# Optimization experiments

Measured on AMD Instinct MI355X. Metric: run time of the kernel, lower is better.

## Reference

```python
import jax, jax.numpy as jnp
import numpy as np

N, E, F, C = 100000, 1600000, 64, 256


def setup_inputs() -> dict:
    key = jax.random.key(0)
    ks = jax.random.split(key, 9)

    def lin(k, fi, fo):
        kw, kb = jax.random.split(k)
        w = jax.random.normal(kw, (fi, fo), jnp.float32) * np.float32(1.0 / np.sqrt(fi))
        b = jax.random.normal(kb, (fo,), jnp.float32) * 0.001
        return w, b

    content = jax.random.normal(ks[0], (N, C), jnp.float32)
    node_emb = jax.random.normal(ks[1], (N + 1, F), jnp.float32) * np.float32(1.0 / (100 * F))
    proj_w, proj_b = lin(ks[2], C, F)
    c0w1, c0b1 = lin(ks[3], 2 * F, 4 * F)   # first layer: inp=2F -> 4F
    c0w2, c0b2 = lin(ks[4], 4 * F, F)
    c1w1, c1b1 = lin(ks[5], 3 * F, 6 * F)   # prediction layer: inp=3F -> 6F
    c1w2, c1b2 = lin(ks[6], 6 * F, F)
    nid = jnp.arange(N, dtype=jnp.int32)
    src = jax.random.randint(ks[7], (E,), 0, N, dtype=jnp.int32)
    dst = jax.random.randint(ks[8], (E,), 0, N, dtype=jnp.int32)
    return dict(content=content, node_emb=node_emb, proj_w=proj_w, proj_b=proj_b,
                c0w1=c0w1, c0b1=c0b1, c0w2=c0w2, c0b2=c0b2,
                c1w1=c1w1, c1b1=c1b1, c1w2=c1w2, c1b2=c1b2,
                nid=nid, src=src, dst=dst)


def _l2norm(x):
    # per-node L2 renorm with clamp(min=1e-6) like torch .norm().clamp
    n = jnp.linalg.norm(x, axis=1, keepdims=True)
    return x / jnp.maximum(n, 1e-6)


def _forward(content, node_emb, proj_w, proj_b,
             c0w1, c0b1, c0w2, c0b2, c1w1, c1b1, c1w2, c1b2,
             nid, src, dst):
    n = content.shape[0]
    lrelu = lambda x: jax.nn.leaky_relu(x, 0.1)
    # node init: embedding + projected content (GaussianNoise is identity in eval)
    h = node_emb[nid + 1] + lrelu(content @ proj_w + proj_b)
    # w = sum of 'one' over in-neighbors = in-degree
    deg = jax.ops.segment_sum(jnp.ones(src.shape[0], h.dtype), dst, num_segments=n)
    wden = jnp.maximum(deg - 1.0, 1.0)[:, None]  # (w - 1).clamp(min=1)

    # ---- layer 0 (first_layer) ----
    h_agg = jax.ops.segment_sum(h[src], dst, num_segments=n)  # copy_src('h') + sum
    h_agg = (h_agg - h) / wden
    z = lrelu(jnp.concatenate([h, h_agg], axis=1) @ c0w1 + c0b1)
    h_new = _l2norm(lrelu(z @ c0w2 + c0b2))
    h_res = _l2norm(h_agg)  # skip is None since in_dims == out_dims
    h = h_new

    # ---- layer 1 (prediction_layer) ----
    h_agg = jax.ops.segment_sum(h[src], dst, num_segments=n)
    h_res_sum = jax.ops.segment_sum(h_res[src], dst, num_segments=n)
    h_agg = (h_agg - h) / wden
    z = lrelu(jnp.concatenate([h, h_agg, h_res_sum], axis=1) @ c1w1 + c1b1)
    h_new = z @ c1w2 + c1b2  # prediction layer: no trailing LeakyReLU
    return _l2norm(h_new)


def reference(content, node_emb, proj_w, proj_b, c0w1, c0b1, c0w2, c0b2,
              c1w1, c1b1, c1w2, c1b2, nid, src, dst):
    return _forward(content, node_emb, proj_w, proj_b,
                    c0w1, c0b1, c0w2, c0b2, c1w1, c1b1, c1w2, c1b2,
                    nid, src, dst)
```

## Files before the change

kernel.cpp:

```cpp
#include <hip/hip_runtime.h>

typedef _Float16 half_t;
typedef half_t h8 __attribute__((ext_vector_type(8)));
typedef float f32x4 __attribute__((ext_vector_type(4)));
typedef unsigned int uint;
typedef unsigned long long ull;
typedef unsigned short ushort;

__device__ __forceinline__ float lrelu_f(float x){ return x >= 0.f ? x : 0.1f*x; }

__device__ __forceinline__ float2 unpack_h2(uint v){
  half_t lo = __builtin_bit_cast(half_t, (unsigned short)(v & 0xffffu));
  half_t hi = __builtin_bit_cast(half_t, (unsigned short)(v >> 16));
  return make_float2((float)lo, (float)hi);
}
__device__ __forceinline__ uint pack_h2(float a, float b){
  unsigned short lo = __builtin_bit_cast(unsigned short, (half_t)a);
  unsigned short hi = __builtin_bit_cast(unsigned short, (half_t)b);
  return (uint)lo | ((uint)hi << 16);
}
__device__ __forceinline__ h8 as_h8(uint4 v){ return __builtin_bit_cast(h8, v); }

enum { EPI_INIT=0, EPI_LRELU=1, EPI_LRELU_L2=2, EPI_L2=3 };
constexpr int CAP = 64;
constexpr int CHUNK = 4096;
constexpr int OSTR = 1056;

__global__ void pack_all_kernel(const float* __restrict__ s0, half_t* __restrict__ d0,
                                const float* __restrict__ s1, half_t* __restrict__ d1,
                                const float* __restrict__ s2, half_t* __restrict__ d2,
                                const float* __restrict__ s3, half_t* __restrict__ d3,
                                const float* __restrict__ s4, half_t* __restrict__ d4){
  int b = blockIdx.x;
  const float* w; half_t* o; int K, M;
  if      (b < 8)  { w=s0; o=d0; K=256; M=64;  }
  else if (b < 24) { w=s1; o=d1; K=128; M=256; b-=8; }
  else if (b < 32) { w=s2; o=d2; K=256; M=64;  b-=24; }
  else if (b < 68) { w=s3; o=d3; K=192; M=384; b-=32; }
  else             { w=s4; o=d4; K=384; M=64;  b-=68; }
  int idx = b*256 + threadIdx.x;
  int total = (K/32)*(M/16)*64;
  if (idx >= total) return;
  int lane = idx & 63;
  int t = idx >> 6;
  int CBn = M/16;
  int cb = t % CBn;
  int s  = t / CBn;
  int k0 = s*32 + (lane>>4)*8;
  int c  = cb*16 + (lane&15);
  #pragma unroll
  for (int j=0;j<8;++j) o[(size_t)idx*8 + j] = (half_t)w[(size_t)(k0+j)*M + c];
}

__global__ __launch_bounds__(256) void binA_kernel(const int* __restrict__ src, const int* __restrict__ dst,
    ull* __restrict__ staging, ushort* __restrict__ offs, int E, int nb){
  __shared__ int hist[1024];
  __shared__ int cursor[1024];
  int c = blockIdx.x;
  int base = c * CHUNK;
  for (int j = threadIdx.x; j < 1024; j += 256) hist[j] = 0;
  __syncthreads();
  #pragma unroll
  for (int it=0; it<CHUNK/256; ++it){
    int i = base + it*256 + threadIdx.x;
    if (i < E) atomicAdd(&hist[dst[i] >> 7], 1);
  }
  __syncthreads();
  for (int off=1; off<1024; off<<=1){
    int v[4];
    #pragma unroll
    for (int k=0;k<4;++k){
      int j = threadIdx.x + k*256;
      v[k] = (j>=off)? hist[j-off] : 0;
    }
    __syncthreads();
    #pragma unroll
    for (int k=0;k<4;++k) hist[threadIdx.x + k*256] += v[k];
    __syncthreads();
  }
  for (int j = threadIdx.x; j < 1024; j += 256){
    int ex = j ? hist[j-1] : 0;
    cursor[j] = ex;
    if (j <= nb) offs[(size_t)c*OSTR + j] = (ushort)ex;
  }
  __syncthreads();
  #pragma unroll
  for (int it=0; it<CHUNK/256; ++it){
    int i = base + it*256 + threadIdx.x;
    if (i < E){
      int d = dst[i];
      int s = src[i];
      int pos = atomicAdd(&cursor[d >> 7], 1);
      staging[(size_t)c*CHUNK + pos] = ((ull)(uint)d << 32) | (uint)s;
    }
  }
}

__global__ __launch_bounds__(256) void scatB_kernel(const ull* __restrict__ staging,
    const ushort* __restrict__ offs, int* __restrict__ cnt, int* __restrict__ col,
    int nChunks, int n){
  __shared__ int lcnt[128];
  int b = blockIdx.x;
  int node0 = b << 7;
  if (threadIdx.x < 128) lcnt[threadIdx.x] = 0;
  __syncthreads();
  for (int c = threadIdx.x; c < nChunks; c += 256){
    const ushort* op = offs + (size_t)c*OSTR;
    int o0 = op[b], o1 = op[b+1];
    const ull* sp = staging + (size_t)c*CHUNK;
    for (int j = o0; j < o1; ++j){
      ull v = sp[j];
      int d = (int)(v >> 32);
      int s = (int)(uint)v;
      int r = atomicAdd(&lcnt[d & 127], 1);
      if (r < CAP) col[(size_t)d*CAP + r] = s;
    }
  }
  __syncthreads();
  if (threadIdx.x < 128){
    int node = node0 + threadIdx.x;
    if (node < n) cnt[node] = lcnt[threadIdx.x];
  }
}

template<int K, int MOUT, int EPI>
__global__ __launch_bounds__(256) void gemm_kernel(
  const float* __restrict__ x0, int st0,
  const half_t* __restrict__ wp, const float* __restrict__ bias,
  half_t* __restrict__ outv, int ost,
  const float* __restrict__ emb, const int* __restrict__ nid, int n)
{
  constexpr int KS = K/32;
  constexpr int CB = MOUT/16;
  const int lane = threadIdx.x & 63;
  const int wid  = threadIdx.x >> 6;
  const int row0 = blockIdx.x*64 + wid*16;
  const int arow = row0 + (lane & 15);
  const int arowc = arow < n ? arow : n-1;
  const int khi = (lane>>4)*8;

  f32x4 areg[2*KS];
  #pragma unroll
  for (int s=0;s<KS;++s){
    int k0 = s*32 + khi;
    areg[2*s]   = *(const f32x4*)(x0 + (size_t)arowc*st0 + k0);
    areg[2*s+1] = *(const f32x4*)(x0 + (size_t)arowc*st0 + k0 + 4);
  }

  f32x4 acc[CB];
  #pragma unroll
  for (int cb=0;cb<CB;++cb) acc[cb] = (f32x4){0.f,0.f,0.f,0.f};

  #pragma unroll
  for (int s=0;s<KS;++s){
    h8 af;
    #pragma unroll
    for (int j=0;j<4;++j){ af[j]=(half_t)areg[2*s][j]; af[j+4]=(half_t)areg[2*s+1][j]; }
    const h8* wrow = (const h8*)wp + (size_t)(s*CB)*64 + lane;
    #pragma unroll
    for (int cb=0;cb<CB;++cb){
      h8 bf = wrow[cb*64];
      acc[cb] = __builtin_amdgcn_mfma_f32_16x16x32_f16(af, bf, acc[cb], 0,0,0);
    }
  }

  const int cgrp = lane >> 4;
  const int ccol = lane & 15;
  #pragma unroll
  for (int r=0;r<4;++r){
    int R = row0 + cgrp*4 + r;
    if (R < n){
      #pragma unroll
      for (int cb=0;cb<CB;++cb){
        float t = lrelu_f(acc[cb][r] + bias[cb*16+ccol]);
        if constexpr (EPI==EPI_INIT) t += emb[(size_t)(nid[R]+1)*64 + cb*16 + ccol];
        outv[(size_t)R*ost + cb*16 + ccol] = (half_t)t;
      }
    }
  }
}

template<int K1, int M1, int M2, int NSRC, int EPI2, bool OUTF16>
__global__ __launch_bounds__(256,4) void mlp_kernel(
  const half_t* __restrict__ x0, const half_t* __restrict__ x1, const half_t* __restrict__ x2,
  int st0, int st1, int st2,
  const half_t* __restrict__ wp1, const float* __restrict__ b1,
  const half_t* __restrict__ wp2, const float* __restrict__ b2,
  void* __restrict__ outv, int ost, int n)
{
  constexpr int RS  = 17;
  constexpr int KS1 = K1/32, CBT = M1/16, CBW = CBT/4;
  constexpr int KS2 = M1/32, CB2 = M2/16;
  constexpr int RED = 65;
  __shared__ uint  zc[M1*RS];
  __shared__ float red[2*16*RED];

  const int lane = threadIdx.x & 63;
  const int wid  = threadIdx.x >> 6;
  const int row0 = blockIdx.x*32;
  const int khi  = (lane>>4)*8;
  const int ccol = lane & 15;
  const int cgrp = lane >> 4;

  f32x4 acc[2][CBW];
  #pragma unroll
  for (int t=0;t<2;++t)
    #pragma unroll
    for (int cb=0;cb<CBW;++cb) acc[t][cb] = (f32x4){0.f,0.f,0.f,0.f};

  #pragma unroll
  for (int s=0;s<KS1;++s){
    int k0 = s*32 + khi;
    const half_t* p = x0; int st = st0; int koff = k0;
    if constexpr (NSRC>1){
      int isrc = k0 >> 6;
      if constexpr (NSRC>=2){ if (isrc==1){ p=x1; st=st1; } }
      if constexpr (NSRC>=3){ if (isrc==2){ p=x2; st=st2; } }
      koff = k0 & 63;
    }
    h8 af[2];
    #pragma unroll
    for (int t=0;t<2;++t){
      int ar = row0 + t*16 + ccol; if (ar >= n) ar = n-1;
      af[t] = *(const h8*)(p + (size_t)ar*st + koff);
    }
    #pragma unroll
    for (int cb=0;cb<CBW;++cb){
      h8 bf = ((const h8*)wp1)[(size_t)(s*CBT + wid*CBW + cb)*64 + lane];
      #pragma unroll
      for (int t=0;t<2;++t)
        acc[t][cb] = __builtin_amdgcn_mfma_f32_16x16x32_f16(af[t], bf, acc[t][cb], 0,0,0);
    }
  }
  #pragma unroll
  for (int t=0;t<2;++t){
    #pragma unroll
    for (int cb=0;cb<CBW;++cb){
      int col = wid*(CBW*16) + cb*16 + ccol;
      float bb = b1[col];
      float v0 = lrelu_f(acc[t][cb][0]+bb);
      float v1 = lrelu_f(acc[t][cb][1]+bb);
      float v2 = lrelu_f(acc[t][cb][2]+bb);
      float v3 = lrelu_f(acc[t][cb][3]+bb);
      int idx = col*RS + t*8 + cgrp*2;
      zc[idx]   = pack_h2(v0,v1);
      zc[idx+1] = pack_h2(v2,v3);
    }
  }
  __syncthreads();

  const int rt = wid & 1, kh = wid >> 1;
  f32x4 acc2[CB2];
  #pragma unroll
  for (int cb=0;cb<CB2;++cb) acc2[cb] = (f32x4){0.f,0.f,0.f,0.f};
  const uint sel = (lane&1) ? 0x07060302u : 0x05040100u;
  const int rp0 = rt*8 + (ccol>>1);

  #pragma unroll
  for (int si=0;si<KS2/2;++si){
    int s = kh*(KS2/2) + si;
    uint v[8];
    #pragma unroll
    for (int j=0;j<8;++j) v[j] = zc[(s*32 + khi + j)*RS + rp0];
    uint4 u;
    u.x = __builtin_amdgcn_perm(v[1], v[0], sel);
    u.y = __builtin_amdgcn_perm(v[3], v[2], sel);
    u.z = __builtin_amdgcn_perm(v[5], v[4], sel);
    u.w = __builtin_amdgcn_perm(v[7], v[6], sel);
    h8 af2 = __builtin_bit_cast(h8, u);
    #pragma unroll
    for (int cb=0;cb<CB2;++cb){
      h8 bf = ((const h8*)wp2)[(size_t)(s*CB2+cb)*64 + lane];
      acc2[cb] = __builtin_amdgcn_mfma_f32_16x16x32_f16(af2, bf, acc2[cb], 0,0,0);
    }
  }
  if (kh == 1){
    #pragma unroll
    for (int cb=0;cb<CB2;++cb)
      #pragma unroll
      for (int r=0;r<4;++r)
        red[(rt*16 + cgrp*4 + r)*RED + cb*16 + ccol] = acc2[cb][r];
  }
  __syncthreads();
  if (kh == 0){
    #pragma unroll
    for (int r=0;r<4;++r){
      int Rr = row0 + rt*16 + cgrp*4 + r;
      float vv[CB2];
      #pragma unroll
      for (int cb=0;cb<CB2;++cb){
        float t = acc2[cb][r] + red[(rt*16 + cgrp*4 + r)*RED + cb*16 + ccol] + b2[cb*16+ccol];
        if constexpr (EPI2==EPI_LRELU_L2) t = lrelu_f(t);
        vv[cb] = t;
      }
      float sq = 0.f;
      #pragma unroll
      for (int cb=0;cb<CB2;++cb) sq += vv[cb]*vv[cb];
      sq += __shfl_xor(sq,1); sq += __shfl_xor(sq,2);
      sq += __shfl_xor(sq,4); sq += __shfl_xor(sq,8);
      float inv = 1.f / fmaxf(sqrtf(sq), 1e-6f);
      if (Rr < n){
        #pragma unroll
        for (int cb=0;cb<CB2;++cb){
          float t = vv[cb]*inv;
          if constexpr (OUTF16)
            ((half_t*)outv)[(size_t)Rr*ost + cb*16 + ccol] = (half_t)t;
          else
            ((float*)outv)[(size_t)Rr*ost + cb*16 + ccol] = t;
        }
      }
    }
  }
}

__global__ __launch_bounds__(256) void segsum0_kernel(const uint* __restrict__ hu, const int* __restrict__ cnt,
                               const int* __restrict__ col,
                               uint* __restrict__ hagg, uint* __restrict__ hc, int n){
  int node = blockIdx.x*4 + (threadIdx.x>>6);
  if (node >= n) return;
  int lane = threadIdx.x & 63;
  int g = lane >> 3, l = lane & 7;
  int deg = cnt[node];
  int degc = deg < CAP ? deg : CAP;
  const int* cv = col + (size_t)node*CAP;
  float a[8] = {0,0,0,0,0,0,0,0};
  int j = g;
  for (; j + 8 < degc; j += 16){
    int c0 = cv[j], c1 = cv[j+8];
    uint4 v0 = *(const uint4*)(hu + (size_t)c0*32 + l*4);
    uint4 v1 = *(const uint4*)(hu + (size_t)c1*32 + l*4);
    h8 s = as_h8(v0) + as_h8(v1);
    #pragma unroll
    for (int q=0;q<8;++q) a[q] += (float)s[q];
  }
  if (j < degc){
    int c = cv[j];
    uint4 v = *(const uint4*)(hu + (size_t)c*32 + l*4);
    h8 s = as_h8(v);
    #pragma unroll
    for (int q=0;q<8;++q) a[q] += (float)s[q];
  }
  #pragma unroll
  for (int q=0;q<8;++q){
    a[q] += __shfl_xor(a[q], 8);
    a[q] += __shfl_xor(a[q], 16);
    a[q] += __shfl_xor(a[q], 32);
  }
  uint4 hv4 = *(const uint4*)(hu + (size_t)node*32 + l*4);
  h8 hvh = as_h8(hv4);
  float iwd = 1.f / fmaxf((float)deg - 1.f, 1.f);
  float sq = 0.f;
  #pragma unroll
  for (int q=0;q<8;++q){ a[q] = (a[q]-(float)hvh[q])*iwd; sq += a[q]*a[q]; }
  sq += __shfl_xor(sq,1); sq += __shfl_xor(sq,2); sq += __shfl_xor(sq,4);
  float inv = 1.f / fmaxf(sqrtf(sq), 1e-6f);
  if (g == 0){
    uint4 oa, oh;
    oa.x = pack_h2(a[0],a[1]); oa.y = pack_h2(a[2],a[3]);
    oa.z = pack_h2(a[4],a[5]); oa.w = pack_h2(a[6],a[7]);
    oh.x = pack_h2(a[0]*inv,a[1]*inv); oh.y = pack_h2(a[2]*inv,a[3]*inv);
    oh.z = pack_h2(a[4]*inv,a[5]*inv); oh.w = pack_h2(a[6]*inv,a[7]*inv);
    *(uint4*)(hagg + (size_t)node*32 + l*4) = oa;
    *(uint4*)(hc + (size_t)node*64 + 32 + l*4) = oh;
  }
}

__global__ __launch_bounds__(256) void segsum1_kernel(const uint* __restrict__ hcu, const int* __restrict__ cnt,
                               const int* __restrict__ col,
                               uint* __restrict__ hagg, uint* __restrict__ hsum, int n){
  int node = blockIdx.x*4 + (threadIdx.x>>6);
  if (node >= n) return;
  int lane = threadIdx.x & 63;
  int g = lane >> 4, l = lane & 15;
  int deg = cnt[node];
  int degc = deg < CAP ? deg : CAP;
  const int* cv = col + (size_t)node*CAP;
  float a[8] = {0,0,0,0,0,0,0,0};
  int j = g;
  for (; j + 12 < degc; j += 16){
    int c0 = cv[j], c1 = cv[j+4], c2 = cv[j+8], c3 = cv[j+12];
    uint4 v0 = *(const uint4*)(hcu + (size_t)c0*64 + l*4);
    uint4 v1 = *(const uint4*)(hcu + (size_t)c1*64 + l*4);
    uint4 v2 = *(const uint4*)(hcu + (size_t)c2*64 + l*4);
    uint4 v3 = *(const uint4*)(hcu + (size_t)c3*64 + l*4);
    h8 s = (as_h8(v0) + as_h8(v1)) + (as_h8(v2) + as_h8(v3));
    #pragma unroll
    for (int q=0;q<8;++q) a[q] += (float)s[q];
  }
  for (; j < degc; j += 4){
    int c = cv[j];
    uint4 v = *(const uint4*)(hcu + (size_t)c*64 + l*4);
    h8 s = as_h8(v);
    #pragma unroll
    for (int q=0;q<8;++q) a[q] += (float)s[q];
  }
  #pragma unroll
  for (int q=0;q<8;++q){
    a[q] += __shfl_xor(a[q], 16);
    a[q] += __shfl_xor(a[q], 32);
  }
  if (g == 0){
    if (l < 8){
      uint4 hv4 = *(const uint4*)(hcu + (size_t)node*64 + l*4);
      h8 hvh = as_h8(hv4);
      float iwd = 1.f / fmaxf((float)deg - 1.f, 1.f);
      uint4 o;
      o.x = pack_h2((a[0]-(float)hvh[0])*iwd,(a[1]-(float)hvh[1])*iwd);
      o.y = pack_h2((a[2]-(float)hvh[2])*iwd,(a[3]-(float)hvh[3])*iwd);
      o.z = pack_h2((a[4]-(float)hvh[4])*iwd,(a[5]-(float)hvh[5])*iwd);
      o.w = pack_h2((a[6]-(float)hvh[6])*iwd,(a[7]-(float)hvh[7])*iwd);
      *(uint4*)(hagg + (size_t)node*32 + l*4) = o;
    } else {
      uint4 o;
      o.x = pack_h2(a[0],a[1]); o.y = pack_h2(a[2],a[3]);
      o.z = pack_h2(a[4],a[5]); o.w = pack_h2(a[6],a[7]);
      *(uint4*)(hsum + (size_t)node*32 + (l-8)*4) = o;
    }
  }
}

extern "C" void kernel_launch(void* const* d_in, const int* in_sizes, int n_in,
                              void* d_out, int out_size, void* d_ws, size_t ws_size,
                              hipStream_t stream){
  const float* content = (const float*)d_in[0];
  const float* node_emb= (const float*)d_in[1];
  const float* proj_w  = (const float*)d_in[2];
  const float* proj_b  = (const float*)d_in[3];
  const float* c0w1 = (const float*)d_in[4];
  const float* c0b1 = (const float*)d_in[5];
  const float* c0w2 = (const float*)d_in[6];
  const float* c0b2 = (const float*)d_in[7];
  const float* c1w1 = (const float*)d_in[8];
  const float* c1b1 = (const float*)d_in[9];
  const float* c1w2 = (const float*)d_in[10];
  const float* c1b2 = (const float*)d_in[11];
  const int* nid = (const int*)d_in[12];
  const int* src = (const int*)d_in[13];
  const int* dst = (const int*)d_in[14];
  float* out = (float*)d_out;
  const int n = in_sizes[12];
  const int E = in_sizes[13];

  char* ws = (char*)d_ws;
  size_t off = 0;
  auto alloc = [&](size_t bytes)->char*{
    char* p = ws + off;
    off = (off + bytes + 255) & ~(size_t)255;
    return p;
  };
  const int nChunks = (E + CHUNK - 1)/CHUNK;
  const int nb = (n + 127) >> 7;
  half_t* h0   = (half_t*)alloc((size_t)n*64*2);
  half_t* hc   = (half_t*)alloc((size_t)n*128*2);
  half_t* hagg0= (half_t*)alloc((size_t)n*64*2);
  half_t* hagg1= (half_t*)alloc((size_t)n*64*2);
  half_t* hsum1= (half_t*)alloc((size_t)n*64*2);
  int* cnt    = (int*)alloc((size_t)n*4);
  int* col    = (int*)alloc((size_t)n*CAP*4);
  ull* staging= (ull*)alloc((size_t)nChunks*CHUNK*8);
  ushort* offs= (ushort*)alloc((size_t)nChunks*OSTR*2);
  half_t* wp0 = (half_t*)alloc((size_t)256*64*2);
  half_t* wp1 = (half_t*)alloc((size_t)128*256*2);
  half_t* wp2 = (half_t*)alloc((size_t)256*64*2);
  half_t* wp3 = (half_t*)alloc((size_t)192*384*2);
  half_t* wp4 = (half_t*)alloc((size_t)384*64*2);

  pack_all_kernel<<<80,256,0,stream>>>(proj_w, wp0, c0w1, wp1, c0w2, wp2, c1w1, wp3, c1w2, wp4);

  binA_kernel<<<nChunks,256,0,stream>>>(src, dst, staging, offs, E, nb);
  scatB_kernel<<<nb,256,0,stream>>>(staging, offs, cnt, col, nChunks, n);

  const int rgrid = (n + 63)/64;
  const int mgrid = (n + 31)/32;

  gemm_kernel<256,64,EPI_INIT><<<rgrid,256,0,stream>>>(
      content, 256, wp0, proj_b, h0, 64, node_emb, nid, n);

  segsum0_kernel<<<(n+3)/4,256,0,stream>>>((const uint*)h0, cnt, col,
                                           (uint*)hagg0, (uint*)hc, n);
  mlp_kernel<128,256,64,2,EPI_LRELU_L2,true><<<mgrid,256,0,stream>>>(
      h0, hagg0, nullptr, 64,64,0, wp1, c0b1, wp2, c0b2, hc, 128, n);

  segsum1_kernel<<<(n+3)/4,256,0,stream>>>((const uint*)hc, cnt, col,
                                           (uint*)hagg1, (uint*)hsum1, n);
  mlp_kernel<192,384,64,3,EPI_L2,false><<<mgrid,256,0,stream>>>(
      hc, hagg1, hsum1, 128,64,64, wp3, c1b1, wp4, c1b2, out, 64, n);
}
```

Measured before the change: 278.1 us.

## Fuse neighbor aggregation into MLP kernels via shared-memory tiles

Removes the two separate segment-sum kernels and performs the neighbor gather and reduction inside each MLP kernel for its 32-row tile. The aggregated rows (and the residual sum in layer 1) go to an LDS tile that overlays the existing reduction buffer, and the first GEMM reads them from there. This drops the global writes and re-reads of hagg0, hagg1 and hsum1, and saves two kernel launches. In exchange, each wave now walks 8 nodes one after another before its MFMA work, which may reduce the parallelism available for the gather.

```diff
diff --git a/kernel.cpp b/kernel.cpp
--- a/kernel.cpp
+++ b/kernel.cpp
@@ -9,11 +9,6 @@
 
 __device__ __forceinline__ float lrelu_f(float x){ return x >= 0.f ? x : 0.1f*x; }
 
-__device__ __forceinline__ float2 unpack_h2(uint v){
-  half_t lo = __builtin_bit_cast(half_t, (unsigned short)(v & 0xffffu));
-  half_t hi = __builtin_bit_cast(half_t, (unsigned short)(v >> 16));
-  return make_float2((float)lo, (float)hi);
-}
 __device__ __forceinline__ uint pack_h2(float a, float b){
   unsigned short lo = __builtin_bit_cast(unsigned short, (half_t)a);
   unsigned short hi = __builtin_bit_cast(unsigned short, (half_t)b);
@@ -180,20 +175,29 @@
   }
 }
 
-template<int K1, int M1, int M2, int NSRC, int EPI2, bool OUTF16>
-__global__ __launch_bounds__(256,4) void mlp_kernel(
-  const half_t* __restrict__ x0, const half_t* __restrict__ x1, const half_t* __restrict__ x2,
-  int st0, int st1, int st2,
+template<int GL, int K1, int M1, int M2, int EPI2, bool OUTF16>
+__global__ __launch_bounds__(256,4) void mlpf_kernel(
+  const half_t* __restrict__ x0, int st0,
+  const uint* __restrict__ gsrc,
+  const int* __restrict__ cnt, const int* __restrict__ col,
   const half_t* __restrict__ wp1, const float* __restrict__ b1,
   const half_t* __restrict__ wp2, const float* __restrict__ b2,
-  void* __restrict__ outv, int ost, int n)
+  void* __restrict__ outv, int ost,
+  uint* __restrict__ hresOut, int n)
 {
   constexpr int RS  = 17;
+  constexpr int RSA = 72;
   constexpr int KS1 = K1/32, CBT = M1/16, CBW = CBT/4;
   constexpr int KS2 = M1/32, CB2 = M2/16;
   constexpr int RED = 65;
+  constexpr int TILEB = (GL==0 ? 1 : 2)*32*RSA*2;
+  constexpr int REDB  = 2*16*RED*4;
+  constexpr int OVLB  = TILEB > REDB ? TILEB : REDB;
   __shared__ uint  zc[M1*RS];
-  __shared__ float red[2*16*RED];
+  __shared__ uint4 ovl[(OVLB+15)/16];
+  half_t* haggT = (half_t*)ovl;
+  half_t* hsumT = (half_t*)ovl + 32*RSA;
+  float*  red   = (float*)ovl;
 
   const int lane = threadIdx.x & 63;
   const int wid  = threadIdx.x >> 6;
@@ -202,6 +206,111 @@
   const int ccol = lane & 15;
   const int cgrp = lane >> 4;
 
+  if constexpr (GL==0){
+    const int g8 = lane >> 3, l8 = lane & 7;
+    for (int pass=0; pass<8; ++pass){
+      int node = row0 + pass*4 + wid;
+      if (node < n){
+        int deg = cnt[node];
+        int degc = deg < CAP ? deg : CAP;
+        const int* cv = col + (size_t)node*CAP;
+        float a[8] = {0,0,0,0,0,0,0,0};
+        int j = g8;
+        for (; j + 8 < degc; j += 16){
+          int c0 = cv[j], c1 = cv[j+8];
+          uint4 v0 = *(const uint4*)(gsrc + (size_t)c0*32 + l8*4);
+          uint4 v1 = *(const uint4*)(gsrc + (size_t)c1*32 + l8*4);
+          h8 s = as_h8(v0) + as_h8(v1);
+          #pragma unroll
+          for (int q=0;q<8;++q) a[q] += (float)s[q];
+        }
+        if (j < degc){
+          uint4 v = *(const uint4*)(gsrc + (size_t)cv[j]*32 + l8*4);
+          h8 s = as_h8(v);
+          #pragma unroll
+          for (int q=0;q<8;++q) a[q] += (float)s[q];
+        }
+        #pragma unroll
+        for (int q=0;q<8;++q){
+          a[q] += __shfl_xor(a[q], 8);
+          a[q] += __shfl_xor(a[q], 16);
+          a[q] += __shfl_xor(a[q], 32);
+        }
+        uint4 hv4 = *(const uint4*)(gsrc + (size_t)node*32 + l8*4);
+        h8 hvh = as_h8(hv4);
+        float iwd = 1.f / fmaxf((float)deg - 1.f, 1.f);
+        float sq = 0.f;
+        #pragma unroll
+        for (int q=0;q<8;++q){ a[q] = (a[q]-(float)hvh[q])*iwd; sq += a[q]*a[q]; }
+        sq += __shfl_xor(sq,1); sq += __shfl_xor(sq,2); sq += __shfl_xor(sq,4);
+        float inv = 1.f / fmaxf(sqrtf(sq), 1e-6f);
+        if (g8 == 0){
+          int lrow = pass*4 + wid;
+          uint4 oa, oh;
+          oa.x = pack_h2(a[0],a[1]); oa.y = pack_h2(a[2],a[3]);
+          oa.z = pack_h2(a[4],a[5]); oa.w = pack_h2(a[6],a[7]);
+          oh.x = pack_h2(a[0]*inv,a[1]*inv); oh.y = pack_h2(a[2]*inv,a[3]*inv);
+          oh.z = pack_h2(a[4]*inv,a[5]*inv); oh.w = pack_h2(a[6]*inv,a[7]*inv);
+          *(uint4*)(haggT + (size_t)lrow*RSA + l8*8) = oa;
+          *(uint4*)(hresOut + (size_t)node*64 + 32 + l8*4) = oh;
+        }
+      }
+    }
+  } else {
+    const int g16 = lane >> 4, l16 = lane & 15;
+    for (int pass=0; pass<8; ++pass){
+      int node = row0 + pass*4 + wid;
+      if (node < n){
+        int deg = cnt[node];
+        int degc = deg < CAP ? deg : CAP;
+        const int* cv = col + (size_t)node*CAP;
+        float a[8] = {0,0,0,0,0,0,0,0};
+        int j = g16;
+        for (; j + 12 < degc; j += 16){
+          int c0 = cv[j], c1 = cv[j+4], c2 = cv[j+8], c3 = cv[j+12];
+          uint4 v0 = *(const uint4*)(gsrc + (size_t)c0*64 + l16*4);
+          uint4 v1 = *(const uint4*)(gsrc + (size_t)c1*64 + l16*4);
+          uint4 v2 = *(const uint4*)(gsrc + (size_t)c2*64 + l16*4);
+          uint4 v3 = *(const uint4*)(gsrc + (size_t)c3*64 + l16*4);
+          h8 s = (as_h8(v0) + as_h8(v1)) + (as_h8(v2) + as_h8(v3));
+          #pragma unroll
+          for (int q=0;q<8;++q) a[q] += (float)s[q];
+        }
+        for (; j < degc; j += 4){
+          uint4 v = *(const uint4*)(gsrc + (size_t)cv[j]*64 + l16*4);
+          h8 s = as_h8(v);
+          #pragma unroll
+          for (int q=0;q<8;++q) a[q] += (float)s[q];
+        }
+        #pragma unroll
+        for (int q=0;q<8;++q){
+          a[q] += __shfl_xor(a[q], 16);
+          a[q] += __shfl_xor(a[q], 32);
+        }
+        if (g16 == 0){
+          int lrow = pass*4 + wid;
+          if (l16 < 8){
+            uint4 hv4 = *(const uint4*)(gsrc + (size_t)node*64 + l16*4);
+            h8 hvh = as_h8(hv4);
+            float iwd = 1.f / fmaxf((float)deg - 1.f, 1.f);
+            uint4 o;
+            o.x = pack_h2((a[0]-(float)hvh[0])*iwd,(a[1]-(float)hvh[1])*iwd);
+            o.y = pack_h2((a[2]-(float)hvh[2])*iwd,(a[3]-(float)hvh[3])*iwd);
+            o.z = pack_h2((a[4]-(float)hvh[4])*iwd,(a[5]-(float)hvh[5])*iwd);
+            o.w = pack_h2((a[6]-(float)hvh[6])*iwd,(a[7]-(float)hvh[7])*iwd);
+            *(uint4*)(haggT + (size_t)lrow*RSA + l16*8) = o;
+          } else {
+            uint4 o;
+            o.x = pack_h2(a[0],a[1]); o.y = pack_h2(a[2],a[3]);
+            o.z = pack_h2(a[4],a[5]); o.w = pack_h2(a[6],a[7]);
+            *(uint4*)(hsumT + (size_t)lrow*RSA + (l16-8)*8) = o;
+          }
+        }
+      }
+    }
+  }
+  __syncthreads();
+
   f32x4 acc[2][CBW];
   #pragma unroll
   for (int t=0;t<2;++t)
@@ -211,18 +320,20 @@
   #pragma unroll
   for (int s=0;s<KS1;++s){
     int k0 = s*32 + khi;
-    const half_t* p = x0; int st = st0; int koff = k0;
-    if constexpr (NSRC>1){
-      int isrc = k0 >> 6;
-      if constexpr (NSRC>=2){ if (isrc==1){ p=x1; st=st1; } }
-      if constexpr (NSRC>=3){ if (isrc==2){ p=x2; st=st2; } }
-      koff = k0 & 63;
-    }
+    int isrc = k0 >> 6;
+    int koff = k0 & 63;
     h8 af[2];
     #pragma unroll
     for (int t=0;t<2;++t){
-      int ar = row0 + t*16 + ccol; if (ar >= n) ar = n-1;
-      af[t] = *(const h8*)(p + (size_t)ar*st + koff);
+      int lr = t*16 + ccol;
+      if (isrc == 0){
+        int ar = row0 + lr; if (ar >= n) ar = n-1;
+        af[t] = *(const h8*)(x0 + (size_t)ar*st0 + koff);
+      } else if (isrc == 1){
+        af[t] = *(const h8*)(haggT + (size_t)lr*RSA + koff);
+      } else {
+        af[t] = *(const h8*)(hsumT + (size_t)lr*RSA + koff);
+      }
     }
     #pragma unroll
     for (int cb=0;cb<CBW;++cb){
@@ -236,13 +347,13 @@
   for (int t=0;t<2;++t){
     #pragma unroll
     for (int cb=0;cb<CBW;++cb){
-      int col = wid*(CBW*16) + cb*16 + ccol;
-      float bb = b1[col];
+      int colx = wid*(CBW*16) + cb*16 + ccol;
+      float bb = b1[colx];
       float v0 = lrelu_f(acc[t][cb][0]+bb);
       float v1 = lrelu_f(acc[t][cb][1]+bb);
       float v2 = lrelu_f(acc[t][cb][2]+bb);
       float v3 = lrelu_f(acc[t][cb][3]+bb);
-      int idx = col*RS + t*8 + cgrp*2;
+      int idx = colx*RS + t*8 + cgrp*2;
       zc[idx]   = pack_h2(v0,v1);
       zc[idx+1] = pack_h2(v2,v3);
     }
@@ -309,112 +420,6 @@
             ((float*)outv)[(size_t)Rr*ost + cb*16 + ccol] = t;
         }
       }
-    }
-  }
-}
-
-__global__ __launch_bounds__(256) void segsum0_kernel(const uint* __restrict__ hu, const int* __restrict__ cnt,
-                               const int* __restrict__ col,
-                               uint* __restrict__ hagg, uint* __restrict__ hc, int n){
-  int node = blockIdx.x*4 + (threadIdx.x>>6);
-  if (node >= n) return;
-  int lane = threadIdx.x & 63;
-  int g = lane >> 3, l = lane & 7;
-  int deg = cnt[node];
-  int degc = deg < CAP ? deg : CAP;
-  const int* cv = col + (size_t)node*CAP;
-  float a[8] = {0,0,0,0,0,0,0,0};
-  int j = g;
-  for (; j + 8 < degc; j += 16){
-    int c0 = cv[j], c1 = cv[j+8];
-    uint4 v0 = *(const uint4*)(hu + (size_t)c0*32 + l*4);
-    uint4 v1 = *(const uint4*)(hu + (size_t)c1*32 + l*4);
-    h8 s = as_h8(v0) + as_h8(v1);
-    #pragma unroll
-    for (int q=0;q<8;++q) a[q] += (float)s[q];
-  }
-  if (j < degc){
-    int c = cv[j];
-    uint4 v = *(const uint4*)(hu + (size_t)c*32 + l*4);
-    h8 s = as_h8(v);
-    #pragma unroll
-    for (int q=0;q<8;++q) a[q] += (float)s[q];
-  }
-  #pragma unroll
-  for (int q=0;q<8;++q){
-    a[q] += __shfl_xor(a[q], 8);
-    a[q] += __shfl_xor(a[q], 16);
-    a[q] += __shfl_xor(a[q], 32);
-  }
-  uint4 hv4 = *(const uint4*)(hu + (size_t)node*32 + l*4);
-  h8 hvh = as_h8(hv4);
-  float iwd = 1.f / fmaxf((float)deg - 1.f, 1.f);
-  float sq = 0.f;
-  #pragma unroll
-  for (int q=0;q<8;++q){ a[q] = (a[q]-(float)hvh[q])*iwd; sq += a[q]*a[q]; }
-  sq += __shfl_xor(sq,1); sq += __shfl_xor(sq,2); sq += __shfl_xor(sq,4);
-  float inv = 1.f / fmaxf(sqrtf(sq), 1e-6f);
-  if (g == 0){
-    uint4 oa, oh;
-    oa.x = pack_h2(a[0],a[1]); oa.y = pack_h2(a[2],a[3]);
-    oa.z = pack_h2(a[4],a[5]); oa.w = pack_h2(a[6],a[7]);
-    oh.x = pack_h2(a[0]*inv,a[1]*inv); oh.y = pack_h2(a[2]*inv,a[3]*inv);
-    oh.z = pack_h2(a[4]*inv,a[5]*inv); oh.w = pack_h2(a[6]*inv,a[7]*inv);
-    *(uint4*)(hagg + (size_t)node*32 + l*4) = oa;
-    *(uint4*)(hc + (size_t)node*64 + 32 + l*4) = oh;
-  }
-}
-
-__global__ __launch_bounds__(256) void segsum1_kernel(const uint* __restrict__ hcu, const int* __restrict__ cnt,
-                               const int* __restrict__ col,
-                               uint* __restrict__ hagg, uint* __restrict__ hsum, int n){
-  int node = blockIdx.x*4 + (threadIdx.x>>6);
-  if (node >= n) return;
-  int lane = threadIdx.x & 63;
-  int g = lane >> 4, l = lane & 15;
-  int deg = cnt[node];
-  int degc = deg < CAP ? deg : CAP;
-  const int* cv = col + (size_t)node*CAP;
-  float a[8] = {0,0,0,0,0,0,0,0};
-  int j = g;
-  for (; j + 12 < degc; j += 16){
-    int c0 = cv[j], c1 = cv[j+4], c2 = cv[j+8], c3 = cv[j+12];
-    uint4 v0 = *(const uint4*)(hcu + (size_t)c0*64 + l*4);
-    uint4 v1 = *(const uint4*)(hcu + (size_t)c1*64 + l*4);
-    uint4 v2 = *(const uint4*)(hcu + (size_t)c2*64 + l*4);
-    uint4 v3 = *(const uint4*)(hcu + (size_t)c3*64 + l*4);
-    h8 s = (as_h8(v0) + as_h8(v1)) + (as_h8(v2) + as_h8(v3));
-    #pragma unroll
-    for (int q=0;q<8;++q) a[q] += (float)s[q];
-  }
-  for (; j < degc; j += 4){
-    int c = cv[j];
-    uint4 v = *(const uint4*)(hcu + (size_t)c*64 + l*4);
-    h8 s = as_h8(v);
-    #pragma unroll
-    for (int q=0;q<8;++q) a[q] += (float)s[q];
-  }
-  #pragma unroll
-  for (int q=0;q<8;++q){
-    a[q] += __shfl_xor(a[q], 16);
-    a[q] += __shfl_xor(a[q], 32);
-  }
-  if (g == 0){
-    if (l < 8){
-      uint4 hv4 = *(const uint4*)(hcu + (size_t)node*64 + l*4);
-      h8 hvh = as_h8(hv4);
-      float iwd = 1.f / fmaxf((float)deg - 1.f, 1.f);
-      uint4 o;
-      o.x = pack_h2((a[0]-(float)hvh[0])*iwd,(a[1]-(float)hvh[1])*iwd);
-      o.y = pack_h2((a[2]-(float)hvh[2])*iwd,(a[3]-(float)hvh[3])*iwd);
-      o.z = pack_h2((a[4]-(float)hvh[4])*iwd,(a[5]-(float)hvh[5])*iwd);
-      o.w = pack_h2((a[6]-(float)hvh[6])*iwd,(a[7]-(float)hvh[7])*iwd);
-      *(uint4*)(hagg + (size_t)node*32 + l*4) = o;
-    } else {
-      uint4 o;
-      o.x = pack_h2(a[0],a[1]); o.y = pack_h2(a[2],a[3]);
-      o.z = pack_h2(a[4],a[5]); o.w = pack_h2(a[6],a[7]);
-      *(uint4*)(hsum + (size_t)node*32 + (l-8)*4) = o;
     }
   }
 }
@@ -452,9 +457,6 @@
   const int nb = (n + 127) >> 7;
   half_t* h0   = (half_t*)alloc((size_t)n*64*2);
   half_t* hc   = (half_t*)alloc((size_t)n*128*2);
-  half_t* hagg0= (half_t*)alloc((size_t)n*64*2);
-  half_t* hagg1= (half_t*)alloc((size_t)n*64*2);
-  half_t* hsum1= (half_t*)alloc((size_t)n*64*2);
   int* cnt    = (int*)alloc((size_t)n*4);
   int* col    = (int*)alloc((size_t)n*CAP*4);
   ull* staging= (ull*)alloc((size_t)nChunks*CHUNK*8);
@@ -476,13 +478,9 @@
   gemm_kernel<256,64,EPI_INIT><<<rgrid,256,0,stream>>>(
       content, 256, wp0, proj_b, h0, 64, node_emb, nid, n);
 
-  segsum0_kernel<<<(n+3)/4,256,0,stream>>>((const uint*)h0, cnt, col,
-                                           (uint*)hagg0, (uint*)hc, n);
-  mlp_kernel<128,256,64,2,EPI_LRELU_L2,true><<<mgrid,256,0,stream>>>(
-      h0, hagg0, nullptr, 64,64,0, wp1, c0b1, wp2, c0b2, hc, 128, n);
-
-  segsum1_kernel<<<(n+3)/4,256,0,stream>>>((const uint*)hc, cnt, col,
-                                           (uint*)hagg1, (uint*)hsum1, n);
-  mlp_kernel<192,384,64,3,EPI_L2,false><<<mgrid,256,0,stream>>>(
-      hc, hagg1, hsum1, 128,64,64, wp3, c1b1, wp4, c1b2, out, 64, n);
-}
+  mlpf_kernel<0,128,256,64,EPI_LRELU_L2,true><<<mgrid,256,0,stream>>>(
+      h0, 64, (const uint*)h0, cnt, col, wp1, c0b1, wp2, c0b2, hc, 128, (uint*)hc, n);
+
+  mlpf_kernel<1,192,384,64,EPI_L2,false><<<mgrid,256,0,stream>>>(
+      hc, 128, (const uint*)hc, cnt, col, wp3, c1b1, wp4, c1b2, out, 64, nullptr, n);
+}
```

Result: slower. 297.1 us (+6.8%).

## Merge weight packing with binning and scatter with input projection GEMM

Applied to the files above, without the earlier changes.

Weight packing and edge binning now run as one launch. The CSR scatter and the content projection GEMM run as another launch, with scatter blocks interleaved every third block among the GEMM blocks. The goal is fewer kernel launches and letting independent work overlap on the GPU. The segment-sum kernels also switch to 32-bit index arithmetic and use v_fma_mix_f32 inline asm to accumulate packed halves straight into fp32, which is meant to cut conversion instructions. The risk is load imbalance inside the fused grids, since scatter blocks are much heavier than GEMM blocks.

```diff
diff --git a/kernel.cpp b/kernel.cpp
--- a/kernel.cpp
+++ b/kernel.cpp
@@ -9,11 +9,6 @@
 
 __device__ __forceinline__ float lrelu_f(float x){ return x >= 0.f ? x : 0.1f*x; }
 
-__device__ __forceinline__ float2 unpack_h2(uint v){
-  half_t lo = __builtin_bit_cast(half_t, (unsigned short)(v & 0xffffu));
-  half_t hi = __builtin_bit_cast(half_t, (unsigned short)(v >> 16));
-  return make_float2((float)lo, (float)hi);
-}
 __device__ __forceinline__ uint pack_h2(float a, float b){
   unsigned short lo = __builtin_bit_cast(unsigned short, (half_t)a);
   unsigned short hi = __builtin_bit_cast(unsigned short, (half_t)b);
@@ -21,42 +16,52 @@
 }
 __device__ __forceinline__ h8 as_h8(uint4 v){ return __builtin_bit_cast(h8, v); }
 
+__device__ __forceinline__ void acc_mix(float& lo, float& hi, uint pk, float one){
+  asm("v_fma_mix_f32 %0, %1, %2, %0 op_sel:[0,0,0] op_sel_hi:[1,0,0]" : "+v"(lo) : "v"(pk), "v"(one));
+  asm("v_fma_mix_f32 %0, %1, %2, %0 op_sel:[1,0,0] op_sel_hi:[1,0,0]" : "+v"(hi) : "v"(pk), "v"(one));
+}
+
 enum { EPI_INIT=0, EPI_LRELU=1, EPI_LRELU_L2=2, EPI_L2=3 };
 constexpr int CAP = 64;
 constexpr int CHUNK = 4096;
 constexpr int OSTR = 1056;
 
-__global__ void pack_all_kernel(const float* __restrict__ s0, half_t* __restrict__ d0,
-                                const float* __restrict__ s1, half_t* __restrict__ d1,
-                                const float* __restrict__ s2, half_t* __restrict__ d2,
-                                const float* __restrict__ s3, half_t* __restrict__ d3,
-                                const float* __restrict__ s4, half_t* __restrict__ d4){
-  int b = blockIdx.x;
-  const float* w; half_t* o; int K, M;
-  if      (b < 8)  { w=s0; o=d0; K=256; M=64;  }
-  else if (b < 24) { w=s1; o=d1; K=128; M=256; b-=8; }
-  else if (b < 32) { w=s2; o=d2; K=256; M=64;  b-=24; }
-  else if (b < 68) { w=s3; o=d3; K=192; M=384; b-=32; }
-  else             { w=s4; o=d4; K=384; M=64;  b-=68; }
-  int idx = b*256 + threadIdx.x;
-  int total = (K/32)*(M/16)*64;
-  if (idx >= total) return;
-  int lane = idx & 63;
-  int t = idx >> 6;
-  int CBn = M/16;
-  int cb = t % CBn;
-  int s  = t / CBn;
-  int k0 = s*32 + (lane>>4)*8;
-  int c  = cb*16 + (lane&15);
-  #pragma unroll
-  for (int j=0;j<8;++j) o[(size_t)idx*8 + j] = (half_t)w[(size_t)(k0+j)*M + c];
-}
-
-__global__ __launch_bounds__(256) void binA_kernel(const int* __restrict__ src, const int* __restrict__ dst,
-    ull* __restrict__ staging, ushort* __restrict__ offs, int E, int nb){
+__global__ __launch_bounds__(256) void front_kernel(
+    const float* __restrict__ s0, half_t* __restrict__ d0,
+    const float* __restrict__ s1, half_t* __restrict__ d1,
+    const float* __restrict__ s2, half_t* __restrict__ d2,
+    const float* __restrict__ s3, half_t* __restrict__ d3,
+    const float* __restrict__ s4, half_t* __restrict__ d4,
+    const int* __restrict__ src, const int* __restrict__ dst,
+    ull* __restrict__ staging, ushort* __restrict__ offs, int E, int nbkt)
+{
   __shared__ int hist[1024];
   __shared__ int cursor[1024];
-  int c = blockIdx.x;
+  int b = blockIdx.x;
+
+  if (b < 80){
+    const float* w; half_t* o; int K, M;
+    if      (b < 8)  { w=s0; o=d0; K=256; M=64;  }
+    else if (b < 24) { w=s1; o=d1; K=128; M=256; b-=8; }
+    else if (b < 32) { w=s2; o=d2; K=256; M=64;  b-=24; }
+    else if (b < 68) { w=s3; o=d3; K=192; M=384; b-=32; }
+    else             { w=s4; o=d4; K=384; M=64;  b-=68; }
+    int idx = b*256 + threadIdx.x;
+    int total = (K/32)*(M/16)*64;
+    if (idx >= total) return;
+    int lane = idx & 63;
+    int t = idx >> 6;
+    int CBn = M/16;
+    int cb = t % CBn;
+    int s  = t / CBn;
+    int k0 = s*32 + (lane>>4)*8;
+    int c  = cb*16 + (lane&15);
+    #pragma unroll
+    for (int j=0;j<8;++j) o[(size_t)idx*8 + j] = (half_t)w[(size_t)(k0+j)*M + c];
+    return;
+  }
+
+  int c = b - 80;
   int base = c * CHUNK;
   for (int j = threadIdx.x; j < 1024; j += 256) hist[j] = 0;
   __syncthreads();
@@ -81,7 +86,7 @@
   for (int j = threadIdx.x; j < 1024; j += 256){
     int ex = j ? hist[j-1] : 0;
     cursor[j] = ex;
-    if (j <= nb) offs[(size_t)c*OSTR + j] = (ushort)ex;
+    if (j <= nbkt) offs[(size_t)c*OSTR + j] = (ushort)ex;
   }
   __syncthreads();
   #pragma unroll
@@ -96,69 +101,73 @@
   }
 }
 
-__global__ __launch_bounds__(256) void scatB_kernel(const ull* __restrict__ staging,
-    const ushort* __restrict__ offs, int* __restrict__ cnt, int* __restrict__ col,
-    int nChunks, int n){
+__global__ __launch_bounds__(256) void mid_kernel(
+    const ull* __restrict__ staging, const ushort* __restrict__ offs,
+    int* __restrict__ cnt, int* __restrict__ col, int nChunks, int nbkt,
+    const float* __restrict__ content, const half_t* __restrict__ wp0,
+    const float* __restrict__ proj_b, const float* __restrict__ node_emb,
+    const int* __restrict__ nid, half_t* __restrict__ h0, int n)
+{
   __shared__ int lcnt[128];
   int b = blockIdx.x;
-  int node0 = b << 7;
-  if (threadIdx.x < 128) lcnt[threadIdx.x] = 0;
-  __syncthreads();
-  for (int c = threadIdx.x; c < nChunks; c += 256){
-    const ushort* op = offs + (size_t)c*OSTR;
-    int o0 = op[b], o1 = op[b+1];
-    const ull* sp = staging + (size_t)c*CHUNK;
-    for (int j = o0; j < o1; ++j){
-      ull v = sp[j];
-      int d = (int)(v >> 32);
-      int s = (int)(uint)v;
-      int r = atomicAdd(&lcnt[d & 127], 1);
-      if (r < CAP) col[(size_t)d*CAP + r] = s;
-    }
-  }
-  __syncthreads();
-  if (threadIdx.x < 128){
-    int node = node0 + threadIdx.x;
-    if (node < n) cnt[node] = lcnt[threadIdx.x];
-  }
-}
-
-template<int K, int MOUT, int EPI>
-__global__ __launch_bounds__(256) void gemm_kernel(
-  const float* __restrict__ x0, int st0,
-  const half_t* __restrict__ wp, const float* __restrict__ bias,
-  half_t* __restrict__ outv, int ost,
-  const float* __restrict__ emb, const int* __restrict__ nid, int n)
-{
-  constexpr int KS = K/32;
-  constexpr int CB = MOUT/16;
+  int m3 = b/3;
+  int scatBefore = (b%3==0) ? m3 : m3+1;
+  if (scatBefore > nbkt) scatBefore = nbkt;
+  bool isScat = (b%3==0) && (m3 < nbkt);
+
+  if (isScat){
+    int bk = m3;
+    int node0 = bk << 7;
+    if (threadIdx.x < 128) lcnt[threadIdx.x] = 0;
+    __syncthreads();
+    for (int c = threadIdx.x; c < nChunks; c += 256){
+      const ushort* op = offs + (size_t)c*OSTR;
+      int o0 = op[bk], o1 = op[bk+1];
+      const ull* sp = staging + (size_t)c*CHUNK;
+      for (int j = o0; j < o1; ++j){
+        ull v = sp[j];
+        int d = (int)(v >> 32);
+        int s = (int)(uint)v;
+        int r = atomicAdd(&lcnt[d & 127], 1);
+        if (r < CAP) col[(size_t)d*CAP + r] = s;
+      }
+    }
+    __syncthreads();
+    if (threadIdx.x < 128){
+      int node = node0 + threadIdx.x;
+      if (node < n) cnt[node] = lcnt[threadIdx.x];
+    }
+    return;
+  }
+
+  int gb = b - scatBefore;
   const int lane = threadIdx.x & 63;
   const int wid  = threadIdx.x >> 6;
-  const int row0 = blockIdx.x*64 + wid*16;
+  const int row0 = gb*64 + wid*16;
   const int arow = row0 + (lane & 15);
   const int arowc = arow < n ? arow : n-1;
   const int khi = (lane>>4)*8;
 
-  f32x4 areg[2*KS];
-  #pragma unroll
-  for (int s=0;s<KS;++s){
-    int k0 = s*32 + khi;
-    areg[2*s]   = *(const f32x4*)(x0 + (size_t)arowc*st0 + k0);
-    areg[2*s+1] = *(const f32x4*)(x0 + (size_t)arowc*st0 + k0 + 4);
-  }
-
-  f32x4 acc[CB];
-  #pragma unroll
-  for (int cb=0;cb<CB;++cb) acc[cb] = (f32x4){0.f,0.f,0.f,0.f};
-
-  #pragma unroll
-  for (int s=0;s<KS;++s){
+  f32x4 areg[16];
+  #pragma unroll
+  for (int s=0;s<8;++s){
+    uint k0 = (uint)arowc*256u + (uint)(s*32 + khi);
+    areg[2*s]   = *(const f32x4*)(content + k0);
+    areg[2*s+1] = *(const f32x4*)(content + k0 + 4);
+  }
+
+  f32x4 acc[4];
+  #pragma unroll
+  for (int cb=0;cb<4;++cb) acc[cb] = (f32x4){0.f,0.f,0.f,0.f};
+
+  #pragma unroll
+  for (int s=0;s<8;++s){
     h8 af;
     #pragma unroll
     for (int j=0;j<4;++j){ af[j]=(half_t)areg[2*s][j]; af[j+4]=(half_t)areg[2*s+1][j]; }
-    const h8* wrow = (const h8*)wp + (size_t)(s*CB)*64 + lane;
-    #pragma unroll
-    for (int cb=0;cb<CB;++cb){
+    const h8* wrow = (const h8*)wp0 + (size_t)(s*4)*64 + lane;
+    #pragma unroll
+    for (int cb=0;cb<4;++cb){
       h8 bf = wrow[cb*64];
       acc[cb] = __builtin_amdgcn_mfma_f32_16x16x32_f16(af, bf, acc[cb], 0,0,0);
     }
@@ -171,10 +180,10 @@
     int R = row0 + cgrp*4 + r;
     if (R < n){
       #pragma unroll
-      for (int cb=0;cb<CB;++cb){
-        float t = lrelu_f(acc[cb][r] + bias[cb*16+ccol]);
-        if constexpr (EPI==EPI_INIT) t += emb[(size_t)(nid[R]+1)*64 + cb*16 + ccol];
-        outv[(size_t)R*ost + cb*16 + ccol] = (half_t)t;
+      for (int cb=0;cb<4;++cb){
+        float t = lrelu_f(acc[cb][r] + proj_b[cb*16+ccol]);
+        t += node_emb[(size_t)(nid[R]+1)*64 + cb*16 + ccol];
+        h0[(size_t)R*64 + cb*16 + ccol] = (half_t)t;
       }
     }
   }
@@ -322,23 +331,23 @@
   int g = lane >> 3, l = lane & 7;
   int deg = cnt[node];
   int degc = deg < CAP ? deg : CAP;
-  const int* cv = col + (size_t)node*CAP;
+  const int* cv = col + ((uint)node<<6);
+  const float one = 1.0f;
   float a[8] = {0,0,0,0,0,0,0,0};
   int j = g;
   for (; j + 8 < degc; j += 16){
-    int c0 = cv[j], c1 = cv[j+8];
-    uint4 v0 = *(const uint4*)(hu + (size_t)c0*32 + l*4);
-    uint4 v1 = *(const uint4*)(hu + (size_t)c1*32 + l*4);
-    h8 s = as_h8(v0) + as_h8(v1);
-    #pragma unroll
-    for (int q=0;q<8;++q) a[q] += (float)s[q];
+    uint c0 = (uint)cv[j], c1 = (uint)cv[j+8];
+    uint4 v0 = *(const uint4*)(hu + (c0<<5) + (l<<2));
+    uint4 v1 = *(const uint4*)(hu + (c1<<5) + (l<<2));
+    uint4 su = __builtin_bit_cast(uint4, as_h8(v0) + as_h8(v1));
+    acc_mix(a[0],a[1],su.x,one); acc_mix(a[2],a[3],su.y,one);
+    acc_mix(a[4],a[5],su.z,one); acc_mix(a[6],a[7],su.w,one);
   }
   if (j < degc){
-    int c = cv[j];
-    uint4 v = *(const uint4*)(hu + (size_t)c*32 + l*4);
-    h8 s = as_h8(v);
-    #pragma unroll
-    for (int q=0;q<8;++q) a[q] += (float)s[q];
+    uint c = (uint)cv[j];
+    uint4 v = *(const uint4*)(hu + (c<<5) + (l<<2));
+    acc_mix(a[0],a[1],v.x,one); acc_mix(a[2],a[3],v.y,one);
+    acc_mix(a[4],a[5],v.z,one); acc_mix(a[6],a[7],v.w,one);
   }
   #pragma unroll
   for (int q=0;q<8;++q){
@@ -346,7 +355,7 @@
     a[q] += __shfl_xor(a[q], 16);
     a[q] += __shfl_xor(a[q], 32);
   }
-  uint4 hv4 = *(const uint4*)(hu + (size_t)node*32 + l*4);
+  uint4 hv4 = *(const uint4*)(hu + ((uint)node<<5) + (l<<2));
   h8 hvh = as_h8(hv4);
   float iwd = 1.f / fmaxf((float)deg - 1.f, 1.f);
   float sq = 0.f;
@@ -360,8 +369,8 @@
     oa.z = pack_h2(a[4],a[5]); oa.w = pack_h2(a[6],a[7]);
     oh.x = pack_h2(a[0]*inv,a[1]*inv); oh.y = pack_h2(a[2]*inv,a[3]*inv);
     oh.z = pack_h2(a[4]*inv,a[5]*inv); oh.w = pack_h2(a[6]*inv,a[7]*inv);
-    *(uint4*)(hagg + (size_t)node*32 + l*4) = oa;
-    *(uint4*)(hc + (size_t)node*64 + 32 + l*4) = oh;
+    *(uint4*)(hagg + ((uint)node<<5) + (l<<2)) = oa;
+    *(uint4*)(hc + ((uint)node<<6) + 32 + (l<<2)) = oh;
   }
 }
 
@@ -374,25 +383,25 @@
   int g = lane >> 4, l = lane & 15;
   int deg = cnt[node];
   int degc = deg < CAP ? deg : CAP;
-  const int* cv = col + (size_t)node*CAP;
+  const int* cv = col + ((uint)node<<6);
+  const float one = 1.0f;
   float a[8] = {0,0,0,0,0,0,0,0};
   int j = g;
   for (; j + 12 < degc; j += 16){
-    int c0 = cv[j], c1 = cv[j+4], c2 = cv[j+8], c3 = cv[j+12];
-    uint4 v0 = *(const uint4*)(hcu + (size_t)c0*64 + l*4);
-    uint4 v1 = *(const uint4*)(hcu + (size_t)c1*64 + l*4);
-    uint4 v2 = *(const uint4*)(hcu + (size_t)c2*64 + l*4);
-    uint4 v3 = *(const uint4*)(hcu + (size_t)c3*64 + l*4);
-    h8 s = (as_h8(v0) + as_h8(v1)) + (as_h8(v2) + as_h8(v3));
-    #pragma unroll
-    for (int q=0;q<8;++q) a[q] += (float)s[q];
+    uint c0 = (uint)cv[j], c1 = (uint)cv[j+4], c2 = (uint)cv[j+8], c3 = (uint)cv[j+12];
+    uint4 v0 = *(const uint4*)(hcu + (c0<<6) + (l<<2));
+    uint4 v1 = *(const uint4*)(hcu + (c1<<6) + (l<<2));
+    uint4 v2 = *(const uint4*)(hcu + (c2<<6) + (l<<2));
+    uint4 v3 = *(const uint4*)(hcu + (c3<<6) + (l<<2));
+    uint4 su = __builtin_bit_cast(uint4, (as_h8(v0) + as_h8(v1)) + (as_h8(v2) + as_h8(v3)));
+    acc_mix(a[0],a[1],su.x,one); acc_mix(a[2],a[3],su.y,one);
+    acc_mix(a[4],a[5],su.z,one); acc_mix(a[6],a[7],su.w,one);
   }
   for (; j < degc; j += 4){
-    int c = cv[j];
-    uint4 v = *(const uint4*)(hcu + (size_t)c*64 + l*4);
-    h8 s = as_h8(v);
-    #pragma unroll
-    for (int q=0;q<8;++q) a[q] += (float)s[q];
+    uint c = (uint)cv[j];
+    uint4 v = *(const uint4*)(hcu + (c<<6) + (l<<2));
+    acc_mix(a[0],a[1],v.x,one); acc_mix(a[2],a[3],v.y,one);
+    acc_mix(a[4],a[5],v.z,one); acc_mix(a[6],a[7],v.w,one);
   }
   #pragma unroll
   for (int q=0;q<8;++q){
@@ -401,7 +410,7 @@
   }
   if (g == 0){
     if (l < 8){
-      uint4 hv4 = *(const uint4*)(hcu + (size_t)node*64 + l*4);
+      uint4 hv4 = *(const uint4*)(hcu + ((uint)node<<6) + (l<<2));
       h8 hvh = as_h8(hv4);
       float iwd = 1.f / fmaxf((float)deg - 1.f, 1.f);
       uint4 o;
@@ -409,12 +418,12 @@
       o.y = pack_h2((a[2]-(float)hvh[2])*iwd,(a[3]-(float)hvh[3])*iwd);
       o.z = pack_h2((a[4]-(float)hvh[4])*iwd,(a[5]-(float)hvh[5])*iwd);
       o.w = pack_h2((a[6]-(float)hvh[6])*iwd,(a[7]-(float)hvh[7])*iwd);
-      *(uint4*)(hagg + (size_t)node*32 + l*4) = o;
+      *(uint4*)(hagg + ((uint)node<<5) + (l<<2)) = o;
     } else {
       uint4 o;
       o.x = pack_h2(a[0],a[1]); o.y = pack_h2(a[2],a[3]);
       o.z = pack_h2(a[4],a[5]); o.w = pack_h2(a[6],a[7]);
-      *(uint4*)(hsum + (size_t)node*32 + (l-8)*4) = o;
+      *(uint4*)(hsum + ((uint)node<<5) + ((l-8)<<2)) = o;
     }
   }
 }
@@ -449,7 +458,7 @@
     return p;
   };
   const int nChunks = (E + CHUNK - 1)/CHUNK;
-  const int nb = (n + 127) >> 7;
+  const int nbkt = (n + 127) >> 7;
   half_t* h0   = (half_t*)alloc((size_t)n*64*2);
   half_t* hc   = (half_t*)alloc((size_t)n*128*2);
   half_t* hagg0= (half_t*)alloc((size_t)n*64*2);
@@ -465,16 +474,16 @@
   half_t* wp3 = (half_t*)alloc((size_t)192*384*2);
   half_t* wp4 = (half_t*)alloc((size_t)384*64*2);
 
-  pack_all_kernel<<<80,256,0,stream>>>(proj_w, wp0, c0w1, wp1, c0w2, wp2, c1w1, wp3, c1w2, wp4);
-
-  binA_kernel<<<nChunks,256,0,stream>>>(src, dst, staging, offs, E, nb);
-  scatB_kernel<<<nb,256,0,stream>>>(staging, offs, cnt, col, nChunks, n);
-
   const int rgrid = (n + 63)/64;
   const int mgrid = (n + 31)/32;
 
-  gemm_kernel<256,64,EPI_INIT><<<rgrid,256,0,stream>>>(
-      content, 256, wp0, proj_b, h0, 64, node_emb, nid, n);
+  front_kernel<<<80 + nChunks, 256, 0, stream>>>(
+      proj_w, wp0, c0w1, wp1, c0w2, wp2, c1w1, wp3, c1w2, wp4,
+      src, dst, staging, offs, E, nbkt);
+
+  mid_kernel<<<nbkt + rgrid, 256, 0, stream>>>(
+      staging, offs, cnt, col, nChunks, nbkt,
+      content, wp0, proj_b, node_emb, nid, h0, n);
 
   segsum0_kernel<<<(n+3)/4,256,0,stream>>>((const uint*)h0, cnt, col,
                                            (uint*)hagg0, (uint*)hc, n);
```

Result: faster. 270.9 us (median of 2 runs) (-2.6%).
